# Performance work log

Measured on AMD Instinct MI355X. Metric: run time of the kernel, lower is better.

Reference implementation:

```python
import jax, jax.numpy as jnp
import numpy as np
import math

EMB_DIM = 1024
N_HEADS = 16
HEAD_DIM = EMB_DIM // N_HEADS
B, T = 4, 2048


def bitlinear(x, w):
    # BitNet b1.58 absmean ternary quantization. NOTE: the source never
    # rescales the ternary weights by `scale`, so forward uses raw {-1,0,1}.
    scale = jnp.maximum(jnp.mean(jnp.abs(w)), 1e-8)
    w_ternary = jnp.clip(jnp.round(w / scale), -1.0, 1.0)
    w_q = w + jax.lax.stop_gradient(w_ternary - w)  # STE
    return x @ w_q.T


def setup_inputs() -> dict:
    key = jax.random.key(0)
    k1, k2, k3 = jax.random.split(key, 3)
    x = jax.random.normal(k1, (B, T, EMB_DIM), dtype=jnp.float32)
    w_qkv = jax.random.normal(k2, (3 * EMB_DIM, EMB_DIM), dtype=jnp.float32) * 0.02
    w_out = jax.random.normal(k3, (EMB_DIM, EMB_DIM), dtype=jnp.float32) * 0.02
    return {"x": x, "w_qkv": w_qkv, "w_out": w_out}


def reference(x, w_qkv, w_out):
    Bc, Tc, C = x.shape
    qkv = bitlinear(x, w_qkv)  # [B, T, 3C]
    q, k, v = jnp.split(qkv, 3, axis=2)

    def split_heads(t):  # [B, T, C] -> [B, H, T, D]
        return t.reshape(Bc, Tc, N_HEADS, HEAD_DIM).transpose(0, 2, 1, 3)

    q, k, v = split_heads(q), split_heads(k), split_heads(v)
    scale = math.sqrt(HEAD_DIM)
    scores = jnp.einsum("bhqd,bhkd->bhqk", q, k) / scale  # [B, H, T, T]
    causal = jnp.triu(jnp.ones((Tc, Tc), dtype=bool), k=1)
    scores = jnp.where(causal, -jnp.inf, scores)
    attn = jax.nn.softmax(scores, axis=-1)
    out = jnp.einsum("bhqk,bhkd->bhqd", attn, v)  # [B, H, T, D]
    out = out.transpose(0, 2, 1, 3).reshape(Bc, Tc, C)
    return bitlinear(out, w_out)
```

## Files before the change

kernel.cpp:

```cpp
#include <hip/hip_runtime.h>
#include <hip/hip_bf16.h>

#define EMB   1024
#define NHEAD 16
#define HDIM  64
#define BSZ   4
#define SEQ   2048
#define MROWS (BSZ*SEQ)
#define NQKV  (3*EMB)

typedef __bf16 bf16;
typedef __bf16 bf16v4 __attribute__((ext_vector_type(4)));
typedef __bf16 bf16v8 __attribute__((ext_vector_type(8)));
typedef float  f32v4  __attribute__((ext_vector_type(4)));
typedef int    i32v4  __attribute__((ext_vector_type(4)));

#define MFMA16(a,b,c)  __builtin_amdgcn_mfma_f32_16x16x32_bf16((a),(b),(c),0,0,0)
#define MFMAI8(a,b,c)  __builtin_amdgcn_mfma_i32_16x16x64_i8((a),(b),(c),0,0,0)

__device__ __forceinline__ void gload_lds16(const void* g, void* l) {
  __builtin_amdgcn_global_load_lds((const __attribute__((address_space(1))) void*)g,
                                   (__attribute__((address_space(3))) void*)l,
                                   16, 0, 0);
}

#define DPP_FMAX(x, ctrl) do {                                                     \
    int _t = __builtin_amdgcn_update_dpp(0, __float_as_int(x), (ctrl), 0xf, 0xf, true); \
    (x) = fmaxf((x), __int_as_float(_t)); } while (0)


__global__ void zero2_kernel(float* p) { p[threadIdx.x] = 0.f; }

__global__ void abs_sum_kernel(const float* __restrict__ w, int n, float* out) {
  float s = 0.f;
  for (int i = blockIdx.x * blockDim.x + threadIdx.x; i < n; i += gridDim.x * blockDim.x)
    s += fabsf(w[i]);
  #pragma unroll
  for (int off = 32; off; off >>= 1) s += __shfl_down(s, off, 64);
  __shared__ float red[4];
  int lane = threadIdx.x & 63, wid = threadIdx.x >> 6;
  if (lane == 0) red[wid] = s;
  __syncthreads();
  if (threadIdx.x == 0) atomicAdd(out, red[0] + red[1] + red[2] + red[3]);
}

__global__ void ternarize_i8_kernel(const float* __restrict__ w, int n,
                                    const float* __restrict__ sum, char* __restrict__ out) {
  int i = blockIdx.x * blockDim.x + threadIdx.x;
  if (i >= n) return;
  float scale = fmaxf(*sum / (float)n, 1e-8f);
  float t = rintf(w[i] / scale);
  t = fmaxf(-1.f, fminf(1.f, t));
  out[i] = (char)(int)t;
}

__global__ void ternarize_bf16_kernel(const float* __restrict__ w, int n,
                                      const float* __restrict__ sum, bf16* __restrict__ out) {
  int i = blockIdx.x * blockDim.x + threadIdx.x;
  if (i >= n) return;
  float scale = fmaxf(*sum / (float)n, 1e-8f);
  float t = rintf(w[i] / scale);
  t = fmaxf(-1.f, fminf(1.f, t));
  out[i] = (bf16)t;
}

__global__ void quant_x_kernel(const float* __restrict__ x, char* __restrict__ p1,
                               char* __restrict__ p2, int n) {
  int i = blockIdx.x * blockDim.x + threadIdx.x;
  if (i >= n) return;
  float v = x[i];
  float q1 = fminf(fmaxf(rintf(v * 16.f), -127.f), 127.f);
  float r = v - q1 * 0.0625f;
  float q2 = fminf(fmaxf(rintf(r * 4096.f), -127.f), 127.f);
  p1[i] = (char)(int)q1;
  p2[i] = (char)(int)q2;
}


__launch_bounds__(256, 2)
__global__ void gemm_qkv_kernel(const char* __restrict__ xq1, const char* __restrict__ xq2,
                                const char* __restrict__ w8,
                                bf16* __restrict__ qh, bf16* __restrict__ ql,
                                bf16* __restrict__ kh, bf16* __restrict__ kl,
                                bf16* __restrict__ vt) {
  __shared__ __align__(16) char A1[128 * 64];
  __shared__ __align__(16) char A2[128 * 64];
  __shared__ __align__(16) char Bs[128 * 64];
  const int tid = threadIdx.x;
  const int lane = tid & 63, wid = tid >> 6;
  const int quad = lane >> 4, l16 = lane & 15;
  const int m0 = blockIdx.x * 128, n0 = blockIdx.y * 128;
  const int wm = (wid >> 1) * 64, wn = (wid & 1) * 64;
  const int asw = (l16 >> 1) & 3;
  i32v4 acc1[4][4] = {};
  i32v4 acc2[4][4] = {};

  for (int kt = 0; kt < EMB / 64; ++kt) {
    __syncthreads();
    #pragma unroll
    for (int r = 0; r < 2; ++r) {
      int li = r * 256 + tid;
      int row = li >> 2, cs = li & 3;
      int cg = cs ^ ((row >> 1) & 3);
      gload_lds16(xq1 + (size_t)(m0 + row) * EMB + kt * 64 + cg * 16, &A1[li * 16]);
      gload_lds16(xq2 + (size_t)(m0 + row) * EMB + kt * 64 + cg * 16, &A2[li * 16]);
      gload_lds16(w8  + (size_t)(n0 + row) * EMB + kt * 64 + cg * 16, &Bs[li * 16]);
    }
    __syncthreads();
    i32v4 af1[4], af2[4], bfr[4];
    #pragma unroll
    for (int i = 0; i < 4; ++i) {
      int arow = wm + i * 16 + l16;
      int off = arow * 64 + ((quad ^ asw) * 16);
      af1[i] = *(const i32v4*)&A1[off];
      af2[i] = *(const i32v4*)&A2[off];
      int brow = wn + i * 16 + l16;
      bfr[i] = *(const i32v4*)&Bs[brow * 64 + ((quad ^ asw) * 16)];
    }
    #pragma unroll
    for (int i = 0; i < 4; ++i)
      #pragma unroll
      for (int j = 0; j < 4; ++j) {
        acc1[i][j] = MFMAI8(af1[i], bfr[j], acc1[i][j]);
        acc2[i][j] = MFMAI8(af2[i], bfr[j], acc2[i][j]);
      }
  }
  const float S1 = 0.0625f, S2 = 1.f / 4096.f;
  const float QSCALE = 0.18033688011112042f;
  #pragma unroll
  for (int i = 0; i < 4; ++i)
    #pragma unroll
    for (int j = 0; j < 4; ++j) {
      const int n = n0 + wn + j * 16 + l16;
      const int region = n >> 10, c1 = n & 1023, h = c1 >> 6, d = c1 & 63;
      const int m_b = m0 + wm + i * 16 + quad * 4;
      float c[4];
      #pragma unroll
      for (int r = 0; r < 4; ++r)
        c[r] = (float)acc1[i][j][r] * S1 + (float)acc2[i][j][r] * S2;
      if (region == 0) {
        #pragma unroll
        for (int r = 0; r < 4; ++r) {
          int m = m_b + r;
          int b = m >> 11, t = m & (SEQ - 1);
          size_t idx = (((size_t)(b * NHEAD + h) * SEQ + t) << 6) + d;
          float cs = c[r] * QSCALE;
          bf16 hi = (bf16)cs;
          qh[idx] = hi; ql[idx] = (bf16)(cs - (float)hi);
        }
      } else if (region == 1) {
        #pragma unroll
        for (int r = 0; r < 4; ++r) {
          int m = m_b + r;
          int b = m >> 11, t = m & (SEQ - 1);
          size_t idx = (((size_t)(b * NHEAD + h) * SEQ + t) << 6) + d;
          bf16 hi = (bf16)c[r];
          kh[idx] = hi; kl[idx] = (bf16)(c[r] - (float)hi);
        }
      } else {
        bf16v4 pk;
        #pragma unroll
        for (int r = 0; r < 4; ++r) pk[r] = (bf16)c[r];
        int b = m_b >> 11, t = m_b & (SEQ - 1);
        *(bf16v4*)&vt[((size_t)(b * NHEAD + h) * HDIM + d) * SEQ + t] = pk;
      }
    }
}


__launch_bounds__(256, 2)
__global__ void attn_kernel(const bf16* __restrict__ qh, const bf16* __restrict__ ql,
                            const bf16* __restrict__ kh, const bf16* __restrict__ kl,
                            const bf16* __restrict__ vt, bf16* __restrict__ o) {
  __shared__ __align__(16) char smem[66560];
  bf16* Qh = (bf16*)smem;
  bf16* Ql = (bf16*)(smem + 16384);
  bf16* Pw = (bf16*)(smem + 49152);
  const int tid = threadIdx.x;
  const int lane = tid & 63, wid = tid >> 6;
  const int quad = lane >> 4, l16 = lane & 15;
  const int xs = l16 & 7;
  const int pair = blockIdx.x;
  const int bh = blockIdx.y;
  const size_t base = (size_t)bh * SEQ * HDIM;

  auto stage_kv = [&](char* dst, int k0) {
    #pragma unroll
    for (int r = 0; r < 2; ++r) {
      int li = r * 256 + tid;
      int srow = li >> 3, scg = (li & 7) ^ (srow & 7);
      gload_lds16(kh + base + (size_t)(k0 + srow) * HDIM + scg * 8, (bf16*)dst + (size_t)li * 8);
      gload_lds16(kl + base + (size_t)(k0 + srow) * HDIM + scg * 8, (bf16*)(dst + 8192) + (size_t)li * 8);
      gload_lds16(vt + base + (size_t)srow * SEQ + k0 + scg * 8,    (bf16*)(dst + 16384) + (size_t)li * 8);
    }
  };

  bf16v8 ones_f;
  {
    bf16 v1 = (l16 == 0) ? (bf16)1.0f : (bf16)0.0f;
    #pragma unroll
    for (int j = 0; j < 8; ++j) ones_f[j] = v1;
  }
  const int b = bh >> 4, h = bh & 15;

  for (int phase = 0; phase < 2; ++phase) {
    const int qt = phase ? (7 - pair) : (8 + pair);
    const int q0 = qt * 128;

    __syncthreads();
    #pragma unroll
    for (int r = 0; r < 4; ++r) {
      int li = r * 256 + tid;
      int row = li >> 3, cg = (li & 7) ^ (row & 7);
      gload_lds16(qh + base + (size_t)(q0 + row) * HDIM + cg * 8, &Qh[li * 8]);
      gload_lds16(ql + base + (size_t)(q0 + row) * HDIM + cg * 8, &Ql[li * 8]);
    }
    __syncthreads();
    bf16v8 qhf[2][2], qlf[2][2];
    #pragma unroll
    for (int sub = 0; sub < 2; ++sub)
      #pragma unroll
      for (int kk = 0; kk < 2; ++kk) {
        int off = (wid * 32 + sub * 16 + l16) * 64 + (((kk << 2) | quad) ^ xs) * 8;
        qhf[sub][kk] = *(const bf16v8*)&Qh[off];
        qlf[sub][kk] = *(const bf16v8*)&Ql[off];
      }
    __syncthreads();

    f32v4 oacc[2][4] = {};
    f32v4 lacc[2] = {};
    float mrow[2][4];
    #pragma unroll
    for (int s = 0; s < 2; ++s)
      #pragma unroll
      for (int r = 0; r < 4; ++r) mrow[s][r] = -1e30f;

    const int qw0 = q0 + wid * 32;
    const int qrow_hi = qw0 + 31;
    const int ntiles = 2 * qt + 2;

    stage_kv(smem, 0);

    for (int ktile = 0; ktile < ntiles; ++ktile) {
      char* cb = smem + (size_t)((ktile & 1) * 24576);
      char* nb = smem + (size_t)(((ktile + 1) & 1) * 24576);
      __syncthreads();
      if (ktile + 1 < ntiles) stage_kv(nb, (ktile + 1) * 64);
      const int k0 = ktile * 64;
      if (k0 > qrow_hi) continue;

      bf16* Kh_ = (bf16*)cb;
      bf16* Kl_ = (bf16*)(cb + 8192);
      bf16* Vt_ = (bf16*)(cb + 16384);

      f32v4 sacc[2][4] = {};
      #pragma unroll
      for (int kk = 0; kk < 2; ++kk) {
        const int co = (((kk << 2) | quad) ^ xs) * 8;
        bf16v8 khf[4], klf[4];
        #pragma unroll
        for (int nt = 0; nt < 4; ++nt) {
          khf[nt] = *(const bf16v8*)&Kh_[(nt * 16 + l16) * 64 + co];
          klf[nt] = *(const bf16v8*)&Kl_[(nt * 16 + l16) * 64 + co];
        }
        #pragma unroll
        for (int sub = 0; sub < 2; ++sub)
          #pragma unroll
          for (int nt = 0; nt < 4; ++nt) {
            sacc[sub][nt] = MFMA16(qhf[sub][kk], khf[nt], sacc[sub][nt]);
            sacc[sub][nt] = MFMA16(qhf[sub][kk], klf[nt], sacc[sub][nt]);
            sacc[sub][nt] = MFMA16(qlf[sub][kk], khf[nt], sacc[sub][nt]);
          }
      }

      #pragma unroll
      for (int sub = 0; sub < 2; ++sub) {
        if (k0 > qw0 + sub * 16 + 15) continue;
        const int qrow_base = qw0 + sub * 16 + quad * 4;
        #pragma unroll
        for (int nt = 0; nt < 4; ++nt) {
          int key = k0 + nt * 16 + l16;
          #pragma unroll
          for (int r = 0; r < 4; ++r)
            if (key > qrow_base + r) sacc[sub][nt][r] = -1e30f;
        }
        float alpha[4];
        #pragma unroll
        for (int r = 0; r < 4; ++r) {
          float mx = fmaxf(fmaxf(sacc[sub][0][r], sacc[sub][1][r]),
                           fmaxf(sacc[sub][2][r], sacc[sub][3][r]));
          DPP_FMAX(mx, 0x128);
          DPP_FMAX(mx, 0x124);
          DPP_FMAX(mx, 0x122);
          DPP_FMAX(mx, 0x121);
          float mnew = fmaxf(mrow[sub][r], mx);
          alpha[r] = __builtin_amdgcn_exp2f(mrow[sub][r] - mnew);
          mrow[sub][r] = mnew;
        }
        bf16* pwave = Pw + (wid * 2 + sub) * (16 * 68);
        #pragma unroll
        for (int nt = 0; nt < 4; ++nt)
          #pragma unroll
          for (int r = 0; r < 4; ++r)
            pwave[(quad * 4 + r) * 68 + nt * 16 + l16] =
                (bf16)__builtin_amdgcn_exp2f(sacc[sub][nt][r] - mrow[sub][r]);
        #pragma unroll
        for (int r = 0; r < 4; ++r) {
          lacc[sub][r] *= alpha[r];
          #pragma unroll
          for (int dt = 0; dt < 4; ++dt) oacc[sub][dt][r] *= alpha[r];
        }
      }

      #pragma unroll
      for (int kk = 0; kk < 2; ++kk) {
        const int co = (((kk << 2) | quad) ^ xs) * 8;
        bf16v8 vf[4];
        #pragma unroll
        for (int dt = 0; dt < 4; ++dt)
          vf[dt] = *(const bf16v8*)&Vt_[(dt * 16 + l16) * 64 + co];
        #pragma unroll
        for (int sub = 0; sub < 2; ++sub) {
          if (k0 > qw0 + sub * 16 + 15) continue;
          bf16v8 pf = *(const bf16v8*)&Pw[(wid * 2 + sub) * (16 * 68) + l16 * 68 + kk * 32 + quad * 8];
          lacc[sub] = MFMA16(pf, ones_f, lacc[sub]);
          #pragma unroll
          for (int dt = 0; dt < 4; ++dt)
            oacc[sub][dt] = MFMA16(pf, vf[dt], oacc[sub][dt]);
        }
      }
    }

    #pragma unroll
    for (int sub = 0; sub < 2; ++sub) {
      float lrow[4];
      #pragma unroll
      for (int r = 0; r < 4; ++r) lrow[r] = __shfl(lacc[sub][r], lane & 48, 64);
      #pragma unroll
      for (int dt = 0; dt < 4; ++dt)
        #pragma unroll
        for (int r = 0; r < 4; ++r) {
          int q = q0 + wid * 32 + sub * 16 + quad * 4 + r;
          int d = dt * 16 + l16;
          float val = oacc[sub][dt][r] / lrow[r];
          o[((size_t)(b * SEQ + q)) * EMB + h * HDIM + d] = (bf16)val;
        }
    }
  }
}


__launch_bounds__(256, 2)
__global__ void gemm_out_kernel(const bf16* __restrict__ oin, const bf16* __restrict__ wt,
                                float* __restrict__ out) {
  __shared__ __align__(16) bf16 As_[128 * 64];
  __shared__ __align__(16) bf16 Bs_[128 * 64];
  const int tid = threadIdx.x;
  const int lane = tid & 63, wid = tid >> 6;
  const int quad = lane >> 4, l16 = lane & 15;
  const int m0 = blockIdx.x * 128, n0 = blockIdx.y * 128;
  const int wm = (wid >> 1) * 64, wn = (wid & 1) * 64;
  f32v4 acc[4][4] = {};

  for (int kt = 0; kt < EMB / 64; ++kt) {
    __syncthreads();
    #pragma unroll
    for (int r = 0; r < 4; ++r) {
      int li = r * 256 + tid;
      int row = li >> 3, col = (li & 7) * 8;
      gload_lds16(oin + (size_t)(m0 + row) * EMB + kt * 64 + col, &As_[li * 8]);
      gload_lds16(wt  + (size_t)(n0 + row) * EMB + kt * 64 + col, &Bs_[li * 8]);
    }
    __syncthreads();
    #pragma unroll
    for (int kk = 0; kk < 2; ++kk) {
      bf16v8 af[4], bfr[4];
      #pragma unroll
      for (int i = 0; i < 4; ++i) {
        af[i]  = *(const bf16v8*)&As_[(wm + i * 16 + l16) * 64 + kk * 32 + quad * 8];
        bfr[i] = *(const bf16v8*)&Bs_[(wn + i * 16 + l16) * 64 + kk * 32 + quad * 8];
      }
      #pragma unroll
      for (int i = 0; i < 4; ++i)
        #pragma unroll
        for (int j = 0; j < 4; ++j)
          acc[i][j] = MFMA16(af[i], bfr[j], acc[i][j]);
    }
  }
  #pragma unroll
  for (int i = 0; i < 4; ++i)
    #pragma unroll
    for (int j = 0; j < 4; ++j)
      #pragma unroll
      for (int r = 0; r < 4; ++r) {
        int m = m0 + wm + i * 16 + quad * 4 + r;
        int n = n0 + wn + j * 16 + l16;
        out[(size_t)m * EMB + n] = acc[i][j][r];
      }
}


extern "C" void kernel_launch(void* const* d_in, const int* in_sizes, int n_in,
                              void* d_out, int out_size, void* d_ws, size_t ws_size,
                              hipStream_t stream) {
  const float* x     = (const float*)d_in[0];
  const float* w_qkv = (const float*)d_in[1];
  const float* w_out = (const float*)d_in[2];
  float* out = (float*)d_out;
  char* ws = (char*)d_ws;

  const size_t SZ  = (size_t)MROWS * EMB * sizeof(bf16);
  const size_t SZ8 = (size_t)MROWS * EMB;
  size_t off = 0;
  float* sums = (float*)ws;            off = 256;
  char*  wq8  = (char*)(ws + off);     off += (size_t)NQKV * EMB;
  bf16*  wo_t = (bf16*)(ws + off);     off += (size_t)EMB * EMB * sizeof(bf16);
  char*  xq1  = (char*)(ws + off);     off += SZ8;
  char*  xq2  = (char*)(ws + off);     off += SZ8;
  bf16*  qh   = (bf16*)(ws + off);     off += SZ;
  bf16*  ql   = (bf16*)(ws + off);     off += SZ;
  bf16*  kh   = (bf16*)(ws + off);     off += SZ;
  bf16*  kl   = (bf16*)(ws + off);     off += SZ;
  bf16*  vt   = (bf16*)(ws + off);     off += SZ;
  bf16*  ob   = (bf16*)xq1;
  (void)in_sizes; (void)n_in; (void)out_size; (void)ws_size;

  zero2_kernel<<<1, 2, 0, stream>>>(sums);
  abs_sum_kernel<<<256, 256, 0, stream>>>(w_qkv, NQKV * EMB, &sums[0]);
  abs_sum_kernel<<<256, 256, 0, stream>>>(w_out, EMB * EMB, &sums[1]);
  ternarize_i8_kernel<<<(NQKV * EMB) / 256, 256, 0, stream>>>(w_qkv, NQKV * EMB, &sums[0], wq8);
  ternarize_bf16_kernel<<<(EMB * EMB) / 256, 256, 0, stream>>>(w_out, EMB * EMB, &sums[1], wo_t);
  quant_x_kernel<<<(MROWS * EMB) / 256, 256, 0, stream>>>(x, xq1, xq2, MROWS * EMB);
  gemm_qkv_kernel<<<dim3(MROWS / 128, NQKV / 128), 256, 0, stream>>>(xq1, xq2, wq8, qh, ql, kh, kl, vt);
  attn_kernel<<<dim3(8, BSZ * NHEAD), 256, 0, stream>>>(qh, ql, kh, kl, vt, ob);
  gemm_out_kernel<<<dim3(MROWS / 128, EMB / 128), 256, 0, stream>>>(ob, wo_t, out);
}
```

Measured before the change: 336.8 us.

## Double-buffer LDS tiles in QKV and output GEMMs to overlap loads with MFMA

Both GEMM kernels now keep two LDS buffers per operand. The next K tile is issued with global_load_lds right after the barrier, while the MFMAs run on the current tile. This also drops one __syncthreads per iteration and aims to hide global memory latency behind compute. It doubles LDS use per block, which could limit occupancy, and the overlap depends on the compiler not forcing an early vmcnt wait.

```diff
diff --git a/kernel.cpp b/kernel.cpp
--- a/kernel.cpp
+++ b/kernel.cpp
@@ -83,9 +83,9 @@
                                 bf16* __restrict__ qh, bf16* __restrict__ ql,
                                 bf16* __restrict__ kh, bf16* __restrict__ kl,
                                 bf16* __restrict__ vt) {
-  __shared__ __align__(16) char A1[128 * 64];
-  __shared__ __align__(16) char A2[128 * 64];
-  __shared__ __align__(16) char Bs[128 * 64];
+  __shared__ __align__(16) char A1[2][128 * 64];
+  __shared__ __align__(16) char A2[2][128 * 64];
+  __shared__ __align__(16) char Bs[2][128 * 64];
   const int tid = threadIdx.x;
   const int lane = tid & 63, wid = tid >> 6;
   const int quad = lane >> 4, l16 = lane & 15;
@@ -95,27 +95,32 @@
   i32v4 acc1[4][4] = {};
   i32v4 acc2[4][4] = {};
 
-  for (int kt = 0; kt < EMB / 64; ++kt) {
-    __syncthreads();
+  auto stage = [&](int bi, int kt) {
     #pragma unroll
     for (int r = 0; r < 2; ++r) {
       int li = r * 256 + tid;
       int row = li >> 2, cs = li & 3;
       int cg = cs ^ ((row >> 1) & 3);
-      gload_lds16(xq1 + (size_t)(m0 + row) * EMB + kt * 64 + cg * 16, &A1[li * 16]);
-      gload_lds16(xq2 + (size_t)(m0 + row) * EMB + kt * 64 + cg * 16, &A2[li * 16]);
-      gload_lds16(w8  + (size_t)(n0 + row) * EMB + kt * 64 + cg * 16, &Bs[li * 16]);
-    }
+      gload_lds16(xq1 + (size_t)(m0 + row) * EMB + kt * 64 + cg * 16, &A1[bi][li * 16]);
+      gload_lds16(xq2 + (size_t)(m0 + row) * EMB + kt * 64 + cg * 16, &A2[bi][li * 16]);
+      gload_lds16(w8  + (size_t)(n0 + row) * EMB + kt * 64 + cg * 16, &Bs[bi][li * 16]);
+    }
+  };
+
+  stage(0, 0);
+  for (int kt = 0; kt < EMB / 64; ++kt) {
+    const int bi = kt & 1;
     __syncthreads();
+    if (kt + 1 < EMB / 64) stage(bi ^ 1, kt + 1);
     i32v4 af1[4], af2[4], bfr[4];
     #pragma unroll
     for (int i = 0; i < 4; ++i) {
       int arow = wm + i * 16 + l16;
       int off = arow * 64 + ((quad ^ asw) * 16);
-      af1[i] = *(const i32v4*)&A1[off];
-      af2[i] = *(const i32v4*)&A2[off];
+      af1[i] = *(const i32v4*)&A1[bi][off];
+      af2[i] = *(const i32v4*)&A2[bi][off];
       int brow = wn + i * 16 + l16;
-      bfr[i] = *(const i32v4*)&Bs[brow * 64 + ((quad ^ asw) * 16)];
+      bfr[i] = *(const i32v4*)&Bs[bi][brow * 64 + ((quad ^ asw) * 16)];
     }
     #pragma unroll
     for (int i = 0; i < 4; ++i)
@@ -353,8 +358,8 @@
 __launch_bounds__(256, 2)
 __global__ void gemm_out_kernel(const bf16* __restrict__ oin, const bf16* __restrict__ wt,
                                 float* __restrict__ out) {
-  __shared__ __align__(16) bf16 As_[128 * 64];
-  __shared__ __align__(16) bf16 Bs_[128 * 64];
+  __shared__ __align__(16) bf16 As_[2][128 * 64];
+  __shared__ __align__(16) bf16 Bs_[2][128 * 64];
   const int tid = threadIdx.x;
   const int lane = tid & 63, wid = tid >> 6;
   const int quad = lane >> 4, l16 = lane & 15;
@@ -362,23 +367,28 @@
   const int wm = (wid >> 1) * 64, wn = (wid & 1) * 64;
   f32v4 acc[4][4] = {};
 
-  for (int kt = 0; kt < EMB / 64; ++kt) {
-    __syncthreads();
+  auto stage = [&](int bi, int kt) {
     #pragma unroll
     for (int r = 0; r < 4; ++r) {
       int li = r * 256 + tid;
       int row = li >> 3, col = (li & 7) * 8;
-      gload_lds16(oin + (size_t)(m0 + row) * EMB + kt * 64 + col, &As_[li * 8]);
-      gload_lds16(wt  + (size_t)(n0 + row) * EMB + kt * 64 + col, &Bs_[li * 8]);
-    }
+      gload_lds16(oin + (size_t)(m0 + row) * EMB + kt * 64 + col, &As_[bi][li * 8]);
+      gload_lds16(wt  + (size_t)(n0 + row) * EMB + kt * 64 + col, &Bs_[bi][li * 8]);
+    }
+  };
+
+  stage(0, 0);
+  for (int kt = 0; kt < EMB / 64; ++kt) {
+    const int bi = kt & 1;
     __syncthreads();
+    if (kt + 1 < EMB / 64) stage(bi ^ 1, kt + 1);
     #pragma unroll
     for (int kk = 0; kk < 2; ++kk) {
       bf16v8 af[4], bfr[4];
       #pragma unroll
       for (int i = 0; i < 4; ++i) {
-        af[i]  = *(const bf16v8*)&As_[(wm + i * 16 + l16) * 64 + kk * 32 + quad * 8];
-        bfr[i] = *(const bf16v8*)&Bs_[(wn + i * 16 + l16) * 64 + kk * 32 + quad * 8];
+        af[i]  = *(const bf16v8*)&As_[bi][(wm + i * 16 + l16) * 64 + kk * 32 + quad * 8];
+        bfr[i] = *(const bf16v8*)&Bs_[bi][(wn + i * 16 + l16) * 64 + kk * 32 + quad * 8];
       }
       #pragma unroll
       for (int i = 0; i < 4; ++i)
```

Result: slower. 349.8 us (+3.9%).
